# Kernel tuning notes

Measured on AMD Instinct MI355X. Metric: run time of the kernel, lower is better.

Reference implementation:

```python
import jax, jax.numpy as jnp
import numpy as np
from jax import lax

BOUNDARY_PER_ITERATION = [3, 2, 1, 0]  # boundary_width=4, boundary_iteration=4


def _cross_dilate(x):
    # grayscale dilation with 3x3 cross structuring element (max over center+4-neighbors)
    p = jnp.pad(x, ((0, 0), (0, 0), (1, 1), (1, 1)), constant_values=-jnp.inf)
    c = p[:, :, 1:-1, 1:-1]
    up = p[:, :, :-2, 1:-1]
    dn = p[:, :, 2:, 1:-1]
    lf = p[:, :, 1:-1, :-2]
    rt = p[:, :, 1:-1, 2:]
    return jnp.maximum(jnp.maximum(jnp.maximum(c, up), jnp.maximum(dn, lf)), rt)


def _full_erode(x):
    # grayscale erosion with full 3x3 structuring element (min over 3x3 window)
    return lax.reduce_window(x, jnp.inf, lax.min, (1, 1, 3, 3), (1, 1, 1, 1),
                             ((0, 0), (0, 0), (1, 1), (1, 1)))


def _box3_sum(x):
    # conv2d with all-ones 3x3 kernel, padding='same'
    return lax.reduce_window(x, 0.0, lax.add, (1, 1, 3, 3), (1, 1, 1, 1),
                             ((0, 0), (0, 0), (1, 1), (1, 1)))


def _find_boundaries(pred_f):
    return (_cross_dilate(pred_f) != _full_erode(pred_f)).astype(pred_f.dtype)


def _expand_boundaries(b, r):
    # dilation with diamond of radius r == r applications of cross dilation
    for _ in range(r):
        b = _cross_dilate(b)
    return b


def _gaussian_kernel_2d(n, std):
    i = np.arange(n, dtype=np.float64) - (n - 1) / 2.0
    g = np.exp(-(i ** 2) / (2.0 * std ** 2))
    g /= g.sum()
    return np.outer(g, g).astype(np.float32)  # cv2.getGaussianKernel outer product


def setup_inputs() -> dict:
    key = jax.random.key(0)
    k1, k2, k3 = jax.random.split(key, 3)
    n, c, h, w = 8, 19, 512, 512
    x = jax.random.normal(k1, (n, c, h, w), dtype=jnp.float32)
    means = jax.random.normal(k2, (c,), dtype=jnp.float32)
    std = jax.random.uniform(k3, (c,), dtype=jnp.float32) + 0.5  # positive variances
    gaussian_kernel = jnp.asarray(_gaussian_kernel_2d(7, 1.0))[None, None]  # (1,1,7,7)
    return {"x": x, "means": means, "std": std, "gaussian_kernel": gaussian_kernel}


def reference(x, means, std, gaussian_kernel):
    # max logits and prediction
    max_logits = jnp.max(x, axis=1, keepdims=True)           # (n,1,h,w)
    pred = jnp.argmax(x, axis=1, keepdims=True)              # (n,1,h,w) int
    sml = (max_logits - means[pred]) / std[pred]             # standardized max logits

    # boundary suppression
    pred_f = pred.astype(sml.dtype)
    boundaries = _find_boundaries(pred_f)
    for r in BOUNDARY_PER_ITERATION:
        expanded = _expand_boundaries(boundaries, r)
        nb_mask = (expanded == 0).astype(sml.dtype)
        sml_masked = sml * nb_mask
        sml_nb = _box3_sum(sml_masked)
        nb_cnt = _box3_sum(nb_mask)
        sml_avg = jnp.where(nb_cnt == 0, sml, sml_nb / jnp.where(nb_cnt == 0, 1.0, nb_cnt))
        sml = jnp.where(nb_mask == 0, sml_avg, sml)

    # dilated smoothing (gaussian conv, padding same)
    sml = lax.conv_general_dilated(sml, gaussian_kernel, (1, 1), 'SAME',
                                   dimension_numbers=('NCHW', 'OIHW', 'NCHW'))
    return sml, pred
```

## Files before the change

### kernel.cpp

```cpp
#include <hip/hip_runtime.h>
#include <cstdint>
#include <cstddef>

#define W_ 512
#define H_ 512
#define N_ 8
#define C_ 19
#define HW_ (W_*H_)
#define NPIX_ (N_*HW_)

#define TS  32
#define SR  46
#define SC  48
#define BR  52

typedef float   f32x4 __attribute__((ext_vector_type(4)));
typedef uint8_t u8x4  __attribute__((ext_vector_type(4)));
typedef unsigned long long u64;

__global__ __launch_bounds__(256) void k_argmax_sml(
    const float* __restrict__ x, const float* __restrict__ means,
    const float* __restrict__ stdv, float* __restrict__ sml,
    uint8_t* __restrict__ pred8, float* __restrict__ predf)
{
    __shared__ float ms[C_], rs[C_];
    const int tid = threadIdx.x;
    if (tid < C_) {
        ms[tid] = means[tid];
        rs[tid] = __builtin_amdgcn_rcpf(stdv[tid]);
    }

    const int seg = blockIdx.x * 4096;
    const int n   = seg >> 18;
    const int p0  = seg & (HW_ - 1);
    const float* base = x + (size_t)n * C_ * HW_ + p0 + 4 * tid;

    f32x4 mv[4];
    int   idx[4][4];
    #pragma unroll
    for (int j = 0; j < 4; ++j) {
        mv[j] = *(const f32x4*)(base + j * 1024);
        idx[j][0] = idx[j][1] = idx[j][2] = idx[j][3] = 0;
    }
    for (int c = 1; c < C_; ++c) {
        const float* bc = base + (size_t)c * HW_;
        #pragma unroll
        for (int j = 0; j < 4; ++j) {
            f32x4 v = *(const f32x4*)(bc + j * 1024);
            #pragma unroll
            for (int k = 0; k < 4; ++k) {
                if (v[k] > mv[j][k]) { mv[j][k] = v[k]; idx[j][k] = c; }
            }
        }
    }
    __syncthreads();
    #pragma unroll
    for (int j = 0; j < 4; ++j) {
        int pix = seg + j * 1024 + 4 * tid;
        f32x4 s, pf; u8x4 pc;
        #pragma unroll
        for (int k = 0; k < 4; ++k) {
            s[k]  = (mv[j][k] - ms[idx[j][k]]) * rs[idx[j][k]];
            pf[k] = (float)idx[j][k];
            pc[k] = (uint8_t)idx[j][k];
        }
        *(f32x4*)(sml + pix) = s;
        *(u8x4*)(pred8 + pix) = pc;
        __builtin_nontemporal_store(pf, (f32x4*)(predf + pix));
    }
}

__global__ __launch_bounds__(256) void k_bnd(
    const uint8_t* __restrict__ pred8, u64* __restrict__ bndM)
{
    int gid  = blockIdx.x * 256 + threadIdx.x;
    int lane = gid & 63;
    int wave = gid >> 6;
    int w = wave & 7;
    int y = (wave >> 3) & 511;
    int n = wave >> 12;
    int xx = w * 64 + lane;
    const uint8_t* pc = pred8 + (size_t)n * HW_ + y * W_ + xx;
    int c = pc[0];
    bool u = y > 0, d = y < H_-1, l = xx > 0, r = xx < W_-1;
    int up = u ? pc[-W_] : c;
    int dn = d ? pc[ W_] : c;
    int lf = l ? pc[-1]  : c;
    int rt = r ? pc[ 1]  : c;
    int mx = max(max(c, up), max(dn, max(lf, rt)));
    int mn = min(min(c, up), min(dn, min(lf, rt)));
    int c00 = (u && l) ? pc[-W_-1] : c;
    int c01 = (u && r) ? pc[-W_+1] : c;
    int c10 = (d && l) ? pc[ W_-1] : c;
    int c11 = (d && r) ? pc[ W_+1] : c;
    mn = min(mn, min(min(c00, c01), min(c10, c11)));
    u64 m = __ballot(mx != mn);
    if (lane == 0) bndM[((size_t)n * 512 + y) * 8 + w] = m;
}

__global__ __launch_bounds__(256) void k_fused(
    const float* __restrict__ sml_g, const u64* __restrict__ bndM,
    const float* __restrict__ gk, float* __restrict__ out)
{
    __shared__ float smlA[SR*SC];
    __shared__ float smlB[SR*SC];
    __shared__ u64 M0[BR], E1[BR], E2[BR], E3[BR], VM[BR];
    __shared__ u64 NBM[4][BR];
    __shared__ float g7[7];
    __shared__ int tACT;

    const int tid = threadIdx.x;
    const int bx = blockIdx.x, by = blockIdx.y, n = blockIdx.z;
    const int tx0 = bx * TS, ty0 = by * TS;
    const float* sg = sml_g + (size_t)n * HW_;

    if (tid == 0) tACT = 0;
    if (tid < 7) g7[tid] = gk[21 + tid] / sqrtf(gk[24]);

    if (tid < BR) {
        int gy = ty0 + tid - 10;
        int bx0 = tx0 - 10;
        u64 m = 0, vm = 0;
        if (gy >= 0 && gy < H_) {
            const u64* row = bndM + ((size_t)n * 512 + gy) * 8;
            int sft = bx0 & 63;
            int wi  = bx0 >> 6;
            u64 w0 = (wi >= 0) ? row[wi] : 0ULL;
            u64 w1 = (wi + 1 <= 7) ? row[wi + 1] : 0ULL;
            m = sft ? ((w0 >> sft) | (w1 << (64 - sft))) : w0;
            int lo = bx0 < 0 ? -bx0 : 0;
            int hi = (512 - bx0) < BR ? (512 - bx0) : BR;
            if (hi > lo) vm = ((1ULL << (hi - lo)) - 1ULL) << lo;
        }
        M0[tid] = m;
        VM[tid] = vm;
    }

    if (bx > 0 && bx < (W_/TS - 1)) {
        for (int s = tid; s < SR * (SC/4); s += 256) {
            int ly = s / (SC/4), j = s - ly * (SC/4);
            int gy = ty0 + ly - 7;
            f32x4 v = {0.f, 0.f, 0.f, 0.f};
            if ((unsigned)gy < (unsigned)H_)
                v = *(const f32x4*)(sg + (size_t)gy * W_ + (tx0 - 8) + j * 4);
            *(f32x4*)&smlA[ly * SC + j * 4] = v;
        }
    } else {
        for (int s = tid; s < SR * SC; s += 256) {
            int ly = s / SC, lx = s - ly * SC;
            int gy = ty0 + ly - 7, gx = tx0 + lx - 8;
            float v = 0.f;
            if ((unsigned)gy < (unsigned)H_ && (unsigned)gx < (unsigned)W_)
                v = sg[(size_t)gy * W_ + gx];
            smlA[ly * SC + lx] = v;
        }
    }
    __syncthreads();

    if (tid < BR) {
        u64 a = M0[tid], u = tid > 0 ? M0[tid-1] : 0, d = tid < BR-1 ? M0[tid+1] : 0;
        E1[tid] = a | (a << 1) | (a >> 1) | u | d;
    }
    __syncthreads();
    if (tid < BR) {
        u64 a = E1[tid], u = tid > 0 ? E1[tid-1] : 0, d = tid < BR-1 ? E1[tid+1] : 0;
        E2[tid] = a | (a << 1) | (a >> 1) | u | d;
    }
    __syncthreads();
    if (tid < BR) {
        u64 a = E2[tid], u = tid > 0 ? E2[tid-1] : 0, d = tid < BR-1 ? E2[tid+1] : 0;
        E3[tid] = a | (a << 1) | (a >> 1) | u | d;
    }
    __syncthreads();
    {
        int r = tid >> 6, i = tid & 63;
        if (i < BR) {
            u64 e = (r == 0) ? M0[i] : (r == 1) ? E1[i] : (r == 2) ? E2[i] : E3[i];
            NBM[r][i] = ~e & VM[i];
        }
    }
    __syncthreads();

    u64 actRow = 0;
    if (tid < SR) {
        int bi = tid + 3;
        u64 U = NBM[0][bi-1] | NBM[0][bi] | NBM[0][bi+1];
        u64 A = (U >> 1) | (U >> 2) | (U >> 3);
        int lo = tx0 == 0 ? 8 : 0;
        int hi = tx0 == (W_-TS) ? 40 : SC;
        u64 CV = (hi - lo >= 64) ? ~0ULL : (((1ULL << (hi - lo)) - 1ULL) << lo);
        actRow = A & CV;
        int gy = ty0 + tid - 7;
        if ((unsigned)gy >= (unsigned)H_) actRow = 0;
        if (actRow) tACT = 1;
    }
    __syncthreads();

    if (tACT) {
        #pragma unroll
        for (int k = 0; k < 4; ++k) {
            const int r = 3 - k;
            const u64 colmask = ((1ULL << (44 - 2*k)) - 1ULL) << (2 + k);
            u64 mwork = 0;
            if (tid >= 1 + k && tid < 45 - k && tid < SR)
                mwork = actRow & colmask;
            u64 mm = mwork;
            while (mm) {
                int lx = __ffsll(mm) - 1; mm &= mm - 1;
                int bi = tid + 3, sh = lx + 1;
                u64 fu = (NBM[r][bi-1] >> sh) & 7ULL;
                u64 fc = (NBM[r][bi  ] >> sh) & 7ULL;
                u64 fd = (NBM[r][bi+1] >> sh) & 7ULL;
                float c = smlA[tid*SC + lx];
                float o;
                if (((fc >> 1) & 1ULL) || !(fu | fc | fd)) {
                    o = c;
                } else {
                    int cnt = __popcll(fu) + __popcll(fc) + __popcll(fd);
                    float sum = 0.f;
                    const float* r0 = &smlA[(tid-1)*SC + lx];
                    const float* r1 = &smlA[(tid  )*SC + lx];
                    const float* r2 = &smlA[(tid+1)*SC + lx];
                    if (fu & 1) sum += r0[-1];
                    if (fu & 2) sum += r0[0];
                    if (fu & 4) sum += r0[1];
                    if (fc & 1) sum += r1[-1];
                    if (fc & 4) sum += r1[1];
                    if (fd & 1) sum += r2[-1];
                    if (fd & 2) sum += r2[0];
                    if (fd & 4) sum += r2[1];
                    o = sum / (float)cnt;
                }
                smlB[tid*SC + lx] = o;
            }
            __syncthreads();
            mm = mwork;
            while (mm) {
                int lx = __ffsll(mm) - 1; mm &= mm - 1;
                smlA[tid*SC + lx] = smlB[tid*SC + lx];
            }
            __syncthreads();
        }
    }

    float* htmp = smlB;
    for (int s = tid; s < 38 * 32; s += 256) {
        int hy = s >> 5, hx = s & 31;
        const float* p = &smlA[(hy + 4)*SC + (hx + 5)];
        htmp[hy*33 + hx] = g7[0]*p[0] + g7[1]*p[1] + g7[2]*p[2] + g7[3]*p[3]
                         + g7[4]*p[4] + g7[5]*p[5] + g7[6]*p[6];
    }
    __syncthreads();
    for (int s = tid; s < TS*TS; s += 256) {
        int oy = s >> 5, ox = s & 31;
        const float* p = &htmp[oy*33 + ox];
        float a = g7[0]*p[0]   + g7[1]*p[33]  + g7[2]*p[66]  + g7[3]*p[99]
                + g7[4]*p[132] + g7[5]*p[165] + g7[6]*p[198];
        out[(size_t)n*HW_ + (size_t)(ty0 + oy)*W_ + (tx0 + ox)] = a;
    }
}

extern "C" void kernel_launch(void* const* d_in, const int* in_sizes, int n_in,
                              void* d_out, int out_size, void* d_ws, size_t ws_size,
                              hipStream_t stream)
{
    const float* x     = (const float*)d_in[0];
    const float* means = (const float*)d_in[1];
    const float* stdv  = (const float*)d_in[2];
    const float* gk    = (const float*)d_in[3];
    float* out_sml  = (float*)d_out;
    float* out_pred = (float*)d_out + NPIX_;

    char* ws = (char*)d_ws;
    float*   sml   = (float*)(ws);
    uint8_t* pred8 = (uint8_t*)(ws + 8388608);
    u64*     bndM  = (u64*)(ws + 10485760);

    k_argmax_sml<<<NPIX_/16/256, 256, 0, stream>>>(x, means, stdv, sml, pred8, out_pred);
    k_bnd<<<NPIX_/256, 256, 0, stream>>>(pred8, bndM);
    dim3 fgrd(W_/TS, H_/TS, N_);
    k_fused<<<fgrd, 256, 0, stream>>>(sml, bndM, gk, out_sml);
}
```

Measured before the change: 55.97 us.

## Stage argmax input tile into LDS via direct global-to-LDS loads

The argmax/standardize kernel now has each block cover 1024 pixels. Its four waves split the 19 channels and bulk-load them straight into shared memory with global_load_lds, then each thread scans all channels from LDS. The goal is more loads in flight at once, where before each thread issued dependent-chain loads across channels from global memory. The cost is 76KB of LDS per block, which limits occupancy, plus four times as many blocks, each doing less work.

```diff
diff --git a/kernel.cpp b/kernel.cpp
--- a/kernel.cpp
+++ b/kernel.cpp
@@ -23,6 +23,7 @@
     const float* __restrict__ stdv, float* __restrict__ sml,
     uint8_t* __restrict__ pred8, float* __restrict__ predf)
 {
+    __shared__ float xs[C_ * 1024];
     __shared__ float ms[C_], rs[C_];
     const int tid = threadIdx.x;
     if (tid < C_) {
@@ -30,44 +31,46 @@
         rs[tid] = __builtin_amdgcn_rcpf(stdv[tid]);
     }
 
-    const int seg = blockIdx.x * 4096;
-    const int n   = seg >> 18;
-    const int p0  = seg & (HW_ - 1);
-    const float* base = x + (size_t)n * C_ * HW_ + p0 + 4 * tid;
-
-    f32x4 mv[4];
-    int   idx[4][4];
+    const int chunk = blockIdx.x;
+    const int n   = chunk >> 8;
+    const int p0  = (chunk & 255) << 10;
+    const int wv  = tid >> 6, lane = tid & 63;
+    const float* xg = x + (size_t)n * C_ * HW_ + p0;
+
+    int cLo = wv * 5;
+    int cHi = cLo + 5 > C_ ? C_ : cLo + 5;
+    for (int c = cLo; c < cHi; ++c) {
+        const float* g = xg + (size_t)c * HW_ + lane * 4;
+        #pragma unroll
+        for (int t = 0; t < 4; ++t) {
+            __builtin_amdgcn_global_load_lds(
+                (const __attribute__((address_space(1))) void*)(g + t * 256),
+                (__attribute__((address_space(3))) void*)&xs[c * 1024 + t * 256],
+                16, 0, 0);
+        }
+    }
+    __syncthreads();
+
+    const f32x4* xv = (const f32x4*)xs;
+    f32x4 mv = xv[tid];
+    int i0 = 0, i1 = 0, i2 = 0, i3 = 0;
     #pragma unroll
-    for (int j = 0; j < 4; ++j) {
-        mv[j] = *(const f32x4*)(base + j * 1024);
-        idx[j][0] = idx[j][1] = idx[j][2] = idx[j][3] = 0;
-    }
     for (int c = 1; c < C_; ++c) {
-        const float* bc = base + (size_t)c * HW_;
-        #pragma unroll
-        for (int j = 0; j < 4; ++j) {
-            f32x4 v = *(const f32x4*)(bc + j * 1024);
-            #pragma unroll
-            for (int k = 0; k < 4; ++k) {
-                if (v[k] > mv[j][k]) { mv[j][k] = v[k]; idx[j][k] = c; }
-            }
-        }
-    }
-    __syncthreads();
-    #pragma unroll
-    for (int j = 0; j < 4; ++j) {
-        int pix = seg + j * 1024 + 4 * tid;
-        f32x4 s, pf; u8x4 pc;
-        #pragma unroll
-        for (int k = 0; k < 4; ++k) {
-            s[k]  = (mv[j][k] - ms[idx[j][k]]) * rs[idx[j][k]];
-            pf[k] = (float)idx[j][k];
-            pc[k] = (uint8_t)idx[j][k];
-        }
-        *(f32x4*)(sml + pix) = s;
-        *(u8x4*)(pred8 + pix) = pc;
-        __builtin_nontemporal_store(pf, (f32x4*)(predf + pix));
-    }
+        f32x4 v = xv[c * 256 + tid];
+        if (v[0] > mv[0]) { mv[0] = v[0]; i0 = c; }
+        if (v[1] > mv[1]) { mv[1] = v[1]; i1 = c; }
+        if (v[2] > mv[2]) { mv[2] = v[2]; i2 = c; }
+        if (v[3] > mv[3]) { mv[3] = v[3]; i3 = c; }
+    }
+    const int pix = chunk * 1024 + tid * 4;
+    f32x4 s, pf; u8x4 pc;
+    s[0] = (mv[0] - ms[i0]) * rs[i0];  pf[0] = (float)i0;  pc[0] = (uint8_t)i0;
+    s[1] = (mv[1] - ms[i1]) * rs[i1];  pf[1] = (float)i1;  pc[1] = (uint8_t)i1;
+    s[2] = (mv[2] - ms[i2]) * rs[i2];  pf[2] = (float)i2;  pc[2] = (uint8_t)i2;
+    s[3] = (mv[3] - ms[i3]) * rs[i3];  pf[3] = (float)i3;  pc[3] = (uint8_t)i3;
+    *(f32x4*)(sml + pix) = s;
+    *(u8x4*)(pred8 + pix) = pc;
+    __builtin_nontemporal_store(pf, (f32x4*)(predf + pix));
 }
 
 __global__ __launch_bounds__(256) void k_bnd(
@@ -276,7 +279,7 @@
     uint8_t* pred8 = (uint8_t*)(ws + 8388608);
     u64*     bndM  = (u64*)(ws + 10485760);
 
-    k_argmax_sml<<<NPIX_/16/256, 256, 0, stream>>>(x, means, stdv, sml, pred8, out_pred);
+    k_argmax_sml<<<NPIX_/1024, 256, 0, stream>>>(x, means, stdv, sml, pred8, out_pred);
     k_bnd<<<NPIX_/256, 256, 0, stream>>>(pred8, bndM);
     dim3 fgrd(W_/TS, H_/TS, N_);
     k_fused<<<fgrd, 256, 0, stream>>>(sml, bndM, gk, out_sml);
```

After: 51.92 us. 7.2% less time.
